# Optimization experiments

Hardware: AMD Instinct MI355X
Metric: run time of the kernel (lower is better)

Reference implementation:

```python
import jax, jax.numpy as jnp
import numpy as np

# model hyperparameters (from init_kwargs)
N_IN = 2048
NN = 512
BATCH = 64
DT, TAU_M, TAU_X = 0.05, 10.0, 2.0
ALPHA = 1.0 - DT / TAU_M   # membrane decay
BETA = 1.0 - DT / TAU_X    # lateral-trace decay
V_TH = 2.0


def _loo_idx(nn):
    # leave-one-out gather indices: idx[j, n] = j if j < n else j + 1
    j = np.arange(nn - 1)[:, None]
    n = np.arange(nn)[None, :]
    return jnp.asarray(j + (j >= n))  # (nn-1, nn) int


def setup_inputs() -> dict:
    key = jax.random.key(0)
    k1, k2, k3, k4 = jax.random.split(key, 4)
    x = jax.random.uniform(k1, (BATCH, N_IN, NN), dtype=jnp.float32)      # per-neuron external input
    v = jax.random.normal(k2, (BATCH, NN), dtype=jnp.float32)             # membrane state
    z = jnp.zeros((BATCH, NN), dtype=jnp.float32)                         # previous spikes
    z_out = jax.random.uniform(k3, (BATCH, NN), dtype=jnp.float32)        # lateral spike trace
    w = jax.random.normal(k4, (N_IN + NN - 1, NN), dtype=jnp.float32) / np.sqrt(N_IN)
    return {"x": x, "v": v, "z": z, "z_out": z_out, "w": w}


def reference(x, v, z, z_out, w):
    # update lateral trace: z_out = beta * z_out + z (z detached in original)
    z_out_new = BETA * z_out + z
    # leave-one-out lateral input: z_loo[b, j, n] = z_out_new[b, j + (j >= n)]
    idx = _loo_idx(NN)
    z_loo = z_out_new[:, idx]  # (B, NN-1, NN)
    # membrane drive: sum_k x_tot[b,k,n] * w[k,n], where x_tot = cat([x, z_loo], dim=1)
    drive = (jnp.einsum('bkn,kn->bn', x, w[:N_IN])
             + jnp.einsum('bjn,jn->bn', z_loo, w[N_IN:]))
    v_new = ALPHA * v + drive - V_TH * z
    # thresholding nonlinearity -> output spikes
    z_new = (v_new - V_TH > 0).astype(v.dtype)
    return v_new, z_new, z_out_new
```

## Files before the change

kernel.cpp:

```cpp
#include <hip/hip_runtime.h>

#define BATCH 64
#define N_IN  2048
#define NN    512
#define G     4
#define ALPHA 0.995f
#define BETA  0.975f
#define V_TH  2.0f

__global__ __launch_bounds__(1024, 8)
void k1_drive1(const float* __restrict__ x,
               const float* __restrict__ w,
               float4* __restrict__ ws)
{
    const int kr  = blockIdx.x;
    const int b0  = blockIdx.y * G;
    const int tid = threadIdx.x;
    const int c4  = tid & 127;
    const int kl  = tid >> 7;

    const float4* __restrict__ x4 = (const float4*)x;
    const float4* __restrict__ w4 = (const float4*)w;
    const int k0 = kr * 64 + kl;

    size_t xoff[G];
#pragma unroll
    for (int g = 0; g < G; ++g)
        xoff[g] = ((size_t)(b0 + g) * N_IN + k0) * 128 + c4;
    size_t woff = (size_t)k0 * 128 + c4;
    const size_t kstep = 8 * 128;

    float4 acc[G];
#pragma unroll
    for (int g = 0; g < G; ++g) acc[g] = make_float4(0.f, 0.f, 0.f, 0.f);

#pragma unroll 2
    for (int i = 0; i < 8; ++i) {
        float4 xv[G];
#pragma unroll
        for (int g = 0; g < G; ++g) xv[g] = x4[xoff[g]];
        const float4 wv = w4[woff];
#pragma unroll
        for (int g = 0; g < G; ++g) {
            acc[g].x += xv[g].x * wv.x;
            acc[g].y += xv[g].y * wv.y;
            acc[g].z += xv[g].z * wv.z;
            acc[g].w += xv[g].w * wv.w;
        }
#pragma unroll
        for (int g = 0; g < G; ++g) xoff[g] += kstep;
        woff += kstep;
    }

    __shared__ float4 red[G][8][128];
#pragma unroll
    for (int g = 0; g < G; ++g) red[g][kl][c4] = acc[g];
    __syncthreads();

    if (tid < 512) {
        const int g = tid >> 7, c = tid & 127;
        float4 s = red[g][0][c];
#pragma unroll
        for (int l = 1; l < 8; ++l) {
            const float4 o = red[g][l][c];
            s.x += o.x; s.y += o.y; s.z += o.z; s.w += o.w;
        }
        ws[((size_t)kr * BATCH + b0 + g) * 128 + c] = s;
    }
}

#define KRF 4
__global__ __launch_bounds__(1024, 8)
void k1_fallback(const float* __restrict__ x,
                 const float* __restrict__ w,
                 float4* __restrict__ ws)
{
    const int nc  = blockIdx.x;
    const int b0  = blockIdx.y * G;
    const int kr  = blockIdx.z;
    const int tid = threadIdx.x;
    const int nl  = tid & 15;
    const int kk  = tid >> 4;
    const int wid  = tid >> 6;
    const int lane = tid & 63;

    const float4* __restrict__ x4 = (const float4*)x;
    const float4* __restrict__ w4 = (const float4*)w;
    const int c4    = nc * 16 + nl;
    const int kbase = kr * 512 + kk;

    size_t xoff[G];
#pragma unroll
    for (int g = 0; g < G; ++g)
        xoff[g] = ((size_t)(b0 + g) * N_IN + kbase) * 128 + c4;
    size_t woff = (size_t)kbase * 128 + c4;

    float4 acc[G];
#pragma unroll
    for (int g = 0; g < G; ++g) acc[g] = make_float4(0.f, 0.f, 0.f, 0.f);

    const size_t kstep = (size_t)64 * 128;
#pragma unroll 2
    for (int i = 0; i < 8; ++i) {
        float4 xv[G];
#pragma unroll
        for (int g = 0; g < G; ++g) xv[g] = x4[xoff[g]];
        const float4 wv = w4[woff];
#pragma unroll
        for (int g = 0; g < G; ++g) {
            acc[g].x += xv[g].x * wv.x;
            acc[g].y += xv[g].y * wv.y;
            acc[g].z += xv[g].z * wv.z;
            acc[g].w += xv[g].w * wv.w;
        }
#pragma unroll
        for (int g = 0; g < G; ++g) xoff[g] += kstep;
        woff += kstep;
    }

#pragma unroll
    for (int off = 32; off >= 16; off >>= 1) {
#pragma unroll
        for (int g = 0; g < G; ++g) {
            acc[g].x += __shfl_down(acc[g].x, off);
            acc[g].y += __shfl_down(acc[g].y, off);
            acc[g].z += __shfl_down(acc[g].z, off);
            acc[g].w += __shfl_down(acc[g].w, off);
        }
    }

    __shared__ float4 wpart[16][G][16];
    if (lane < 16) {
#pragma unroll
        for (int g = 0; g < G; ++g) wpart[wid][g][lane] = acc[g];
    }
    __syncthreads();

    if (tid < 64) {
        const int g = tid >> 4, c = tid & 15;
        float4 s = wpart[0][g][c];
#pragma unroll
        for (int ww = 1; ww < 16; ++ww) {
            const float4 o = wpart[ww][g][c];
            s.x += o.x; s.y += o.y; s.z += o.z; s.w += o.w;
        }
        ws[((size_t)kr * BATCH + b0 + g) * 128 + nc * 16 + c] = s;
    }
}

template <int KRV>
__global__ __launch_bounds__(1024)
void k2_finish(const float* __restrict__ v,
               const float* __restrict__ z,
               const float* __restrict__ z_out,
               const float* __restrict__ w,
               const float* __restrict__ ws,
               float* __restrict__ out)
{
    const int nc  = blockIdx.x;
    const int b   = blockIdx.y;
    const int nb  = nc * 64;
    const int tid = threadIdx.x;

    __shared__ float zlds[NN];
    __shared__ float r2[1024];

    if (tid < NN)
        zlds[tid] = BETA * z_out[b * NN + tid] + z[b * NN + tid];
    __syncthreads();

    const int n_loc = tid & 63;
    const int n     = nb + n_loc;
    const int jg    = tid >> 6;
    float d2 = 0.f;
#pragma unroll 4
    for (int j = jg; j < NN - 1; j += 16)
        d2 += zlds[j + (j >= n)] * w[(size_t)(N_IN + j) * NN + n];
    r2[tid] = d2;
    __syncthreads();

    if (tid < 64) {
        float d1 = 0.f;
#pragma unroll
        for (int kr = 0; kr < KRV; ++kr)
            d1 += ws[((size_t)kr * BATCH + b) * NN + n];
        float d2s = 0.f;
#pragma unroll
        for (int g = 0; g < 16; ++g) d2s += r2[g * 64 + n_loc];
        const float vv    = v[b * NN + n];
        const float zz    = z[b * NN + n];
        const float v_new = ALPHA * vv + d1 + d2s - V_TH * zz;
        out[b * NN + n]                  = v_new;
        out[BATCH * NN + b * NN + n]     = (v_new - V_TH > 0.f) ? 1.f : 0.f;
        out[2 * BATCH * NN + b * NN + n] = zlds[n];
    }
}

extern "C" void kernel_launch(void* const* d_in, const int* in_sizes, int n_in,
                              void* d_out, int out_size, void* d_ws, size_t ws_size,
                              hipStream_t stream) {
    (void)in_sizes; (void)n_in; (void)out_size;
    const float* x     = (const float*)d_in[0];
    const float* v     = (const float*)d_in[1];
    const float* z     = (const float*)d_in[2];
    const float* z_out = (const float*)d_in[3];
    const float* w     = (const float*)d_in[4];
    float* out = (float*)d_out;
    float* wsf = (float*)d_ws;

    const size_t need32 = (size_t)32 * BATCH * NN * sizeof(float);
    if (ws_size >= need32) {
        dim3 g1(32, BATCH / G);
        k1_drive1<<<g1, 1024, 0, stream>>>(x, w, (float4*)wsf);
        dim3 g2(8, BATCH);
        k2_finish<32><<<g2, 1024, 0, stream>>>(v, z, z_out, w, wsf, out);
    } else {
        dim3 g1(8, BATCH / G, KRF);
        k1_fallback<<<g1, 1024, 0, stream>>>(x, w, (float4*)wsf);
        dim3 g2(8, BATCH);
        k2_finish<KRF><<<g2, 1024, 0, stream>>>(v, z, z_out, w, wsf, out);
    }
}
```

Measured before the change: 53.49 us.

## Fuse leave-one-out lateral term into split-K kernel and slim epilogue

```diff
diff --git a/kernel.cpp b/kernel.cpp
--- a/kernel.cpp
+++ b/kernel.cpp
@@ -9,10 +9,11 @@
 #define V_TH  2.0f
 
 __global__ __launch_bounds__(1024, 8)
-void k1_drive1(const float* __restrict__ x,
-               const float* __restrict__ w,
+void k1_stream(const float* __restrict__ x, const float* __restrict__ w,
+               const float* __restrict__ z, const float* __restrict__ z_out,
                float4* __restrict__ ws)
 {
+    __shared__ __align__(16) float4 red[G][8][128];
     const int kr  = blockIdx.x;
     const int b0  = blockIdx.y * G;
     const int tid = threadIdx.x;
@@ -52,27 +53,80 @@
         woff += kstep;
     }
 
-    __shared__ float4 red[G][8][128];
 #pragma unroll
     for (int g = 0; g < G; ++g) red[g][kl][c4] = acc[g];
     __syncthreads();
 
+    float4 s = make_float4(0.f, 0.f, 0.f, 0.f);
     if (tid < 512) {
         const int g = tid >> 7, c = tid & 127;
-        float4 s = red[g][0][c];
+        s = red[g][0][c];
 #pragma unroll
         for (int l = 1; l < 8; ++l) {
             const float4 o = red[g][l][c];
             s.x += o.x; s.y += o.y; s.z += o.z; s.w += o.w;
         }
+    }
+    __syncthreads();
+
+    float* d2l = (float*)red;
+    float* zr  = d2l + G * NN;
+    const int j0 = kr * 16;
+
+    if (tid < G * 17) {
+        const int g = tid / 17, jj = tid % 17;
+        const int idx = j0 + jj;
+        if (idx < NN)
+            zr[g * 17 + jj] = BETA * z_out[(b0 + g) * NN + idx]
+                            + z[(b0 + g) * NN + idx];
+    }
+    __syncthreads();
+
+    {
+        const int n  = tid & 511;
+        const int gh = tid >> 9;
+        float p0 = 0.f, p1 = 0.f;
+        const int jend = (j0 + 16 < NN - 1) ? j0 + 16 : NN - 1;
+        for (int j = j0; j < jend; ++j) {
+            const float wv = w[(size_t)(N_IN + j) * NN + n];
+            const int jj = j + (j >= n) - j0;
+            p0 += zr[(gh * 2 + 0) * 17 + jj] * wv;
+            p1 += zr[(gh * 2 + 1) * 17 + jj] * wv;
+        }
+        d2l[(gh * 2 + 0) * NN + n] = p0;
+        d2l[(gh * 2 + 1) * NN + n] = p1;
+    }
+    __syncthreads();
+
+    if (tid < 512) {
+        const int g = tid >> 7, c = tid & 127;
+        s.x += d2l[g * NN + 4 * c + 0];
+        s.y += d2l[g * NN + 4 * c + 1];
+        s.z += d2l[g * NN + 4 * c + 2];
+        s.w += d2l[g * NN + 4 * c + 3];
         ws[((size_t)kr * BATCH + b0 + g) * 128 + c] = s;
     }
 }
 
-#define KRF 4
+__global__ __launch_bounds__(128)
+void k3_epi(const float* __restrict__ v, const float* __restrict__ z,
+            const float* __restrict__ z_out, const float* __restrict__ ws,
+            float* __restrict__ out)
+{
+    const int i = blockIdx.x * 128 + threadIdx.x;
+    float d = 0.f;
+#pragma unroll
+    for (int kr = 0; kr < 32; ++kr)
+        d += ws[(size_t)kr * (BATCH * NN) + i];
+    const float zz = z[i];
+    const float vn = ALPHA * v[i] + d - V_TH * zz;
+    out[i]                  = vn;
+    out[BATCH * NN + i]     = (vn - V_TH > 0.f) ? 1.f : 0.f;
+    out[2 * BATCH * NN + i] = BETA * z_out[i] + zz;
+}
+
 __global__ __launch_bounds__(1024, 8)
-void k1_fallback(const float* __restrict__ x,
-                 const float* __restrict__ w,
+void k1_fallback(const float* __restrict__ x, const float* __restrict__ w,
                  float4* __restrict__ ws)
 {
     const int nc  = blockIdx.x;
@@ -94,12 +148,12 @@
     for (int g = 0; g < G; ++g)
         xoff[g] = ((size_t)(b0 + g) * N_IN + kbase) * 128 + c4;
     size_t woff = (size_t)kbase * 128 + c4;
+    const size_t kstep = (size_t)64 * 128;
 
     float4 acc[G];
 #pragma unroll
     for (int g = 0; g < G; ++g) acc[g] = make_float4(0.f, 0.f, 0.f, 0.f);
 
-    const size_t kstep = (size_t)64 * 128;
 #pragma unroll 2
     for (int i = 0; i < 8; ++i) {
         float4 xv[G];
@@ -138,24 +192,20 @@
 
     if (tid < 64) {
         const int g = tid >> 4, c = tid & 15;
-        float4 s = wpart[0][g][c];
+        float4 sf = wpart[0][g][c];
 #pragma unroll
         for (int ww = 1; ww < 16; ++ww) {
             const float4 o = wpart[ww][g][c];
-            s.x += o.x; s.y += o.y; s.z += o.z; s.w += o.w;
-        }
-        ws[((size_t)kr * BATCH + b0 + g) * 128 + nc * 16 + c] = s;
-    }
-}
-
-template <int KRV>
+            sf.x += o.x; sf.y += o.y; sf.z += o.z; sf.w += o.w;
+        }
+        ws[((size_t)kr * BATCH + b0 + g) * 128 + nc * 16 + c] = sf;
+    }
+}
+
 __global__ __launch_bounds__(1024)
-void k2_finish(const float* __restrict__ v,
-               const float* __restrict__ z,
-               const float* __restrict__ z_out,
-               const float* __restrict__ w,
-               const float* __restrict__ ws,
-               float* __restrict__ out)
+void k2_finish(const float* __restrict__ v, const float* __restrict__ z,
+               const float* __restrict__ z_out, const float* __restrict__ w,
+               const float* __restrict__ ws, float* __restrict__ out)
 {
     const int nc  = blockIdx.x;
     const int b   = blockIdx.y;
@@ -182,7 +232,7 @@
     if (tid < 64) {
         float d1 = 0.f;
 #pragma unroll
-        for (int kr = 0; kr < KRV; ++kr)
+        for (int kr = 0; kr < 4; ++kr)
             d1 += ws[((size_t)kr * BATCH + b) * NN + n];
         float d2s = 0.f;
 #pragma unroll
@@ -211,13 +261,12 @@
     const size_t need32 = (size_t)32 * BATCH * NN * sizeof(float);
     if (ws_size >= need32) {
         dim3 g1(32, BATCH / G);
-        k1_drive1<<<g1, 1024, 0, stream>>>(x, w, (float4*)wsf);
-        dim3 g2(8, BATCH);
-        k2_finish<32><<<g2, 1024, 0, stream>>>(v, z, z_out, w, wsf, out);
+        k1_stream<<<g1, 1024, 0, stream>>>(x, w, z, z_out, (float4*)wsf);
+        k3_epi<<<BATCH * NN / 128, 128, 0, stream>>>(v, z, z_out, wsf, out);
     } else {
-        dim3 g1(8, BATCH / G, KRF);
+        dim3 g1(8, BATCH / G, 4);
         k1_fallback<<<g1, 1024, 0, stream>>>(x, w, (float4*)wsf);
         dim3 g2(8, BATCH);
-        k2_finish<KRF><<<g2, 1024, 0, stream>>>(v, z, z_out, w, wsf, out);
-    }
-}
+        k2_finish<<<g2, 1024, 0, stream>>>(v, z, z_out, w, wsf, out);
+    }
+}
```

New measurement: 49.73 us, median of 2. 7.0% less time.
